# Optimization experiments

Hardware: AMD Instinct MI355X
Metric: run time of the kernel (lower is better)

## Reference

```python
import jax, jax.numpy as jnp
import numpy as np

N_QUBITS = 14
N_LAYERS = 4
BATCH = 2048
DIM = 2 ** N_QUBITS


def setup_inputs() -> dict:
    key = jax.random.key(0)
    k1, k2 = jax.random.split(key)
    x = jax.random.normal(k1, (BATCH, N_QUBITS), dtype=jnp.float32)
    params = 2.0 * jnp.pi * jax.random.uniform(k2, (N_LAYERS, 1, N_QUBITS), dtype=jnp.float32)
    return {"x": x, "params": params}


def _angle_embed_x(x):
    """RX(x_q) angle embedding from |0...0>: product state, qubit 0 most significant."""
    B, n = x.shape
    c = jnp.cos(x / 2)
    s = jnp.sin(x / 2)
    state = jnp.ones((B, 1), dtype=jnp.complex64)
    for q in range(n):  # fixed small loop over qubits (kron build-up)
        amp = jnp.stack([c[:, q] + 0j, (-1j) * s[:, q]], axis=-1).astype(jnp.complex64)  # (B,2)
        state = (state[:, :, None] * amp[:, None, :]).reshape(B, -1)
    return state  # (B, 2^n)


def _apply_rx(state, theta, q, n):
    """Apply RX(theta) on qubit q to batched state (B, 2^n)."""
    c = jnp.cos(theta / 2).astype(jnp.complex64)
    s = ((-1j) * jnp.sin(theta / 2)).astype(jnp.complex64)
    B = state.shape[0]
    st = state.reshape(B, 2 ** q, 2, 2 ** (n - q - 1))
    a0, a1 = st[:, :, 0, :], st[:, :, 1, :]
    new = jnp.stack([c * a0 + s * a1, s * a0 + c * a1], axis=2)
    return new.reshape(B, -1)


def _apply_cnot(state, ctrl, tgt, n):
    B = state.shape[0]
    lo, hi = min(ctrl, tgt), max(ctrl, tgt)
    st = state.reshape(B, 2 ** lo, 2, 2 ** (hi - lo - 1), 2, 2 ** (n - hi - 1))
    if ctrl < tgt:
        # control axis=2, target axis=4: flip target where control==1
        flipped = st[:, :, 1, :, ::-1, :]
        st = jnp.stack([st[:, :, 0], flipped], axis=2)
    else:
        # control axis=4, target axis=2
        flipped = st[:, :, ::-1, :, 1, :]
        st = jnp.stack([st[:, :, :, :, 0, :], flipped], axis=4)
    return st.reshape(B, -1)


def _z_signs(n):
    # sign[q, k] = +1 if bit q (MSB-first) of k is 0 else -1
    k = np.arange(2 ** n)
    bits = (k[None, :] >> np.arange(n - 1, -1, -1)[:, None]) & 1
    return jnp.asarray(1.0 - 2.0 * bits, dtype=jnp.float32)  # (n, 2^n)


def reference(x, params):
    n = N_QUBITS
    state = _angle_embed_x(x)  # (B, 2^n) complex64
    for layer in range(N_LAYERS):
        w = params[layer, 0]  # (n,)
        for q in range(n):
            state = _apply_rx(state, w[q], q, n)
        for q in range(n):  # ring of CNOTs (basic entangling layer)
            state = _apply_cnot(state, q, (q + 1) % n, n)
    probs = state.real ** 2 + state.imag ** 2  # (B, 2^n)
    return probs @ _z_signs(n).T  # (B, n) per-qubit <Z>
```

## Files before the change

### kernel.cpp

```cpp
#include <hip/hip_runtime.h>
#include <hip/hip_fp16.h>

#define NQ     14
#define NL     4
#define BATCH  2048
#define DIM    16384
#define BLK    512
#define NCH    (DIM / 4)
#define PCH    (NCH + NCH / 8)

using f2 = __attribute__((ext_vector_type(2))) float;
__device__ __forceinline__ f2 ff2(float a, float b) { f2 r; r.x = a; r.y = b; return r; }

__device__ __forceinline__ unsigned h2u(__half2 h) { return __builtin_bit_cast(unsigned, h); }
__device__ __forceinline__ __half2 u2h(unsigned u) { return __builtin_bit_cast(__half2, u); }
__device__ __forceinline__ unsigned sw16(unsigned u) { return __builtin_amdgcn_alignbit(u, u, 16); }

template <int K>
__device__ __forceinline__ void rot_k(__half2* X, __half2* Y, __half2 T, __half2 Sn) {
#pragma unroll
  for (int k = 0; k < 16; ++k) {
    if (!(k & K)) {
      const int k1 = k | K;
      const __half2 u1 = __hfma2(T, Y[k1], X[k]);
      const __half2 w1 = __hfma2(Sn, u1, Y[k1]);
      X[k]  = __hfma2(T, w1, u1);
      Y[k1] = w1;
      const __half2 u2 = __hfma2(T, Y[k], X[k1]);
      const __half2 w2 = __hfma2(Sn, u2, Y[k]);
      X[k1] = __hfma2(T, w2, u2);
      Y[k]  = w2;
    }
  }
}
__device__ __forceinline__ void rot0(__half2* X, __half2* Y, __half2 T, __half2 Sn) {
#pragma unroll
  for (int k = 0; k < 16; ++k) {
    const __half2 sy = __lowhigh2highlow(Y[k]);
    const __half2 u = __hfma2(T, sy, X[k]);
    const __half2 w = __hfma2(Sn, u, sy);
    X[k] = __hfma2(T, w, u);
    Y[k] = __lowhigh2highlow(w);
  }
}

__device__ __forceinline__ void cnot_scatter(char* sb, const int* offD, int P,
                                             const __half2* X, const __half2* Y) {
#pragma unroll
  for (int g = 0; g < 8; ++g) {
    const int k0 = 2 * g;
    const unsigned w0 = __builtin_amdgcn_perm(h2u(X[k0 ^ 12]), h2u(X[k0]), 0x07060100u);
    const unsigned w1 = __builtin_amdgcn_perm(h2u(Y[k0 ^ 12]), h2u(Y[k0]), 0x07060100u);
    const unsigned w2 = __builtin_amdgcn_perm(h2u(X[k0 ^ 13]), h2u(X[k0 ^ 1]), 0x05040302u);
    const unsigned w3 = __builtin_amdgcn_perm(h2u(Y[k0 ^ 13]), h2u(Y[k0 ^ 1]), 0x05040302u);
    const bool rev = ((P ^ (__popc(g) & 1)) != 0);
    const uint4 o = make_uint4(rev ? sw16(w2) : w0, rev ? sw16(w3) : w1,
                               rev ? sw16(w0) : w2, rev ? sw16(w1) : w3);
    *(uint4*)(sb + offD[g]) = o;
  }
}

__global__ __launch_bounds__(BLK)
__attribute__((amdgpu_waves_per_eu(4, 4)))
void qsim_kernel(const float* __restrict__ x,
                 const float* __restrict__ params,
                 float* __restrict__ out) {
  __shared__ uint4 lds[PCH];
  __shared__ float exc[NQ], exs[NQ];
  __shared__ uint2 gTS[NL * NQ];
  __shared__ float red[8][16];
  char* const sb = (char*)lds;

  const int b = blockIdx.x;
  const int t = threadIdx.x;

  if (t < NQ) {
    const float xv = x[b * NQ + t] + params[t];
    exc[t] = cosf(0.5f * xv); exs[t] = sinf(0.5f * xv);
  }
  if (t >= NQ && t < NL * NQ) {
    float ph = 0.5f * params[t];
    if (ph > 1.5707964f) ph -= 3.14159265f;
    const float tf = tanf(0.5f * ph);
    const __half th = __float2half_rn(tf);
    const float thf = __half2float(th);
    const float sf = 2.0f * thf / (1.0f + thf * thf);
    gTS[t] = make_uint2(h2u(__half2half2(th)), h2u(__float2half2_rn(-sf)));
  }
  __syncthreads();

  __half2 X[16], Y[16];

  char* const pA = sb + 16 * (9 * t);
  char* const pB = sb + 16 * (t & 7) + 1152 * (t >> 3);
  char* const pC = sb + 16 * ((t & 63) + ((t >> 3) & 7) + 576 * (t >> 6));
  char* const pD = sb + 16 * (t + (t >> 3));

  int MA0 = 0;
  {
    const int Me[9] = {0x2007, 0x200F, 0x201F, 0x203F, 0x207F, 0x20FF, 0x21FF, 0x23FF, 0x27FF};
#pragma unroll
    for (int i = 0; i < 9; ++i) if ((t >> i) & 1) MA0 ^= Me[i];
  }
  int offD[8];
#pragma unroll
  for (int g = 0; g < 8; ++g) {
    const int Mrep = ((g & 1) ? 0x2FFF : 0) ^ ((g & 2) ? 0x3FFF : 0) ^ ((g & 4) ? 0x1FFF : 0);
    const int cT = (MA0 ^ Mrep) >> 2;
    offD[g] = 16 * (cT + (cT >> 3));
  }
  const int P = __popc(t) & 1;

  {
    float pb = 1.0f;
#pragma unroll
    for (int i = 0; i < 9; ++i) pb *= ((t >> i) & 1) ? exs[11 - i] : exc[11 - i];
    const int pct = __popc(t);
#pragma unroll
    for (int m = 0; m < 8; ++m) {
      const float fm = ((m & 1) ? exs[2] : exc[2]) * ((m & 2) ? exs[1] : exc[1]) *
                       ((m & 4) ? exs[0] : exc[0]);
      float xv[4], yv[4];
#pragma unroll
      for (int l = 0; l < 4; ++l) {
        const float fl = ((l & 1) ? exs[13] : exc[13]) * ((l & 2) ? exs[12] : exc[12]);
        const float f = pb * fm * fl;
        const int pc = (pct + __popc(m) + __popc(l)) & 3;
        xv[l] = (pc == 0) ? f : ((pc == 2) ? -f : 0.0f);
        yv[l] = (pc == 1) ? -f : ((pc == 3) ? f : 0.0f);
      }
      X[2 * m]     = __floats2half2_rn(xv[0], xv[1]);
      X[2 * m + 1] = __floats2half2_rn(xv[2], xv[3]);
      Y[2 * m]     = __floats2half2_rn(yv[0], yv[1]);
      Y[2 * m + 1] = __floats2half2_rn(yv[2], yv[3]);
    }
  }
  cnot_scatter(sb, offD, P, X, Y);
  __syncthreads();

#pragma unroll
  for (int layer = 1; layer < NL; ++layer) {
    __half2 T, Sn;
#define MKST(qi) { const uint2 g_ = gTS[layer * NQ + (qi)]; T = u2h(g_.x); Sn = u2h(g_.y); }

#pragma unroll
    for (int i = 0; i < 8; ++i) {
      const uint4 u = *(const uint4*)(pA + 16 * i);
      X[2 * i] = u2h(u.x); Y[2 * i] = u2h(u.y);
      X[2 * i + 1] = u2h(u.z); Y[2 * i + 1] = u2h(u.w);
    }
    MKST(13); rot0(X, Y, T, Sn);
    MKST(12); rot_k<1>(X, Y, T, Sn);
    MKST(11); rot_k<2>(X, Y, T, Sn);
    MKST(10); rot_k<4>(X, Y, T, Sn);
    MKST(9);  rot_k<8>(X, Y, T, Sn);
#pragma unroll
    for (int i = 0; i < 8; ++i)
      *(uint4*)(pA + 16 * i) = make_uint4(h2u(X[2 * i]), h2u(Y[2 * i]),
                                          h2u(X[2 * i + 1]), h2u(Y[2 * i + 1]));
    __builtin_amdgcn_wave_barrier();

#pragma unroll
    for (int m = 0; m < 8; ++m) {
      const uint4 u = *(const uint4*)(pB + 144 * m);
      X[2 * m] = u2h(u.x); Y[2 * m] = u2h(u.y);
      X[2 * m + 1] = u2h(u.z); Y[2 * m + 1] = u2h(u.w);
    }
    MKST(8); rot_k<2>(X, Y, T, Sn);
    MKST(7); rot_k<4>(X, Y, T, Sn);
    MKST(6); rot_k<8>(X, Y, T, Sn);
#pragma unroll
    for (int m = 0; m < 8; ++m)
      *(uint4*)(pB + 144 * m) = make_uint4(h2u(X[2 * m]), h2u(Y[2 * m]),
                                           h2u(X[2 * m + 1]), h2u(Y[2 * m + 1]));
    __builtin_amdgcn_wave_barrier();

#pragma unroll
    for (int m = 0; m < 8; ++m) {
      const uint4 u = *(const uint4*)(pC + 1152 * m);
      X[2 * m] = u2h(u.x); Y[2 * m] = u2h(u.y);
      X[2 * m + 1] = u2h(u.z); Y[2 * m + 1] = u2h(u.w);
    }
    MKST(5); rot_k<2>(X, Y, T, Sn);
    MKST(4); rot_k<4>(X, Y, T, Sn);
    MKST(3); rot_k<8>(X, Y, T, Sn);
#pragma unroll
    for (int m = 0; m < 8; ++m)
      *(uint4*)(pC + 1152 * m) = make_uint4(h2u(X[2 * m]), h2u(Y[2 * m]),
                                            h2u(X[2 * m + 1]), h2u(Y[2 * m + 1]));
    __syncthreads();

#pragma unroll
    for (int m = 0; m < 8; ++m) {
      const uint4 u = *(const uint4*)(pD + 9216 * m);
      X[2 * m] = u2h(u.x); Y[2 * m] = u2h(u.y);
      X[2 * m + 1] = u2h(u.z); Y[2 * m + 1] = u2h(u.w);
    }
    if (layer < NL - 1) __syncthreads();
    MKST(2); rot_k<2>(X, Y, T, Sn);
    MKST(1); rot_k<4>(X, Y, T, Sn);
    MKST(0); rot_k<8>(X, Y, T, Sn);
#undef MKST

    if (layer < NL - 1) {
      cnot_scatter(sb, offD, P, X, Y);
      __syncthreads();
    }
  }

  {
    f2 pp[16];
#pragma unroll
    for (int k = 0; k < 16; ++k) {
      const float xl = __low2float(X[k]), xh = __high2float(X[k]);
      const float yl = __low2float(Y[k]), yh = __high2float(Y[k]);
      pp[k] = ff2(fmaf(xl, xl, yl * yl), fmaf(xh, xh, yh * yh));
    }
#pragma unroll
    for (int st = 0; st < 4; ++st) {
      const int h = 1 << st;
#pragma unroll
      for (int k = 0; k < 16; ++k) {
        if (!(k & h)) {
          const f2 u = pp[k], w = pp[k | h];
          pp[k] = u + w;
          pp[k | h] = u - w;
        }
      }
    }
    float w24 = pp[12].x + pp[12].y;
    float w28 = pp[14].x + pp[14].y;
    float w30 = pp[15].x + pp[15].y;
    float w31 = pp[15].x - pp[15].y;
    float w15 = pp[7].x - pp[7].y;

    const int lane = t & 63;
#pragma unroll
    for (int m = 0; m < 6; ++m) {
      const int h = 1 << m;
      const bool hi = (lane & h) != 0;
      float u;
      u = __shfl_xor(w28, h, 64); w28 = hi ? (u - w28) : (u + w28);
      u = __shfl_xor(w30, h, 64); w30 = hi ? (u - w30) : (u + w30);
      u = __shfl_xor(w31, h, 64); w31 = hi ? (u - w31) : (u + w31);
      u = __shfl_xor(w15, h, 64); w15 = hi ? (u - w15) : (u + w15);
      u = __shfl_xor(w24, h, 64); w24 = u + w24;
    }
    const int w = t >> 6;
    const float swv = (__popc(w) & 1) ? -1.0f : 1.0f;
    if (lane == 0) {
      red[w][1] = w24;
      red[w][2] = w28;
      red[w][3] = ((w >> 2) & 1) ? -w28 : w28;
      red[w][4] = (((w >> 1) ^ (w >> 2)) & 1) ? -w28 : w28;
      red[w][5] = swv * w28;
    } else if (lane == 32) { red[w][6]  = swv * w28; }
    else if (lane == 48)   { red[w][7]  = swv * w28; }
    else if (lane == 56)   { red[w][8]  = swv * w28; }
    else if (lane == 60)   { red[w][9]  = swv * w28; }
    else if (lane == 62)   { red[w][10] = swv * w28; }
    else if (lane == 63)   { red[w][11] = swv * w28;
                             red[w][12] = swv * w30;
                             red[w][13] = swv * w31;
                             red[w][0]  = swv * w15; }
    __syncthreads();
    if (t < NQ) {
      float sq = 0.0f;
#pragma unroll
      for (int ww = 0; ww < 8; ++ww) sq += red[ww][t];
      out[b * NQ + t] = sq;
    }
  }
}

extern "C" void kernel_launch(void* const* d_in, const int* in_sizes, int n_in,
                              void* d_out, int out_size, void* d_ws, size_t ws_size,
                              hipStream_t stream) {
  const float* x      = (const float*)d_in[0];
  const float* params = (const float*)d_in[1];
  float* out          = (float*)d_out;
  qsim_kernel<<<BATCH, BLK, 0, stream>>>(x, params, out);
}
```

Measured before the change: 163.3 us.

## Replace per-qubit RX half2 rotations with grouped-qubit MFMA unitary matmuls

A small prep kernel builds fused 32x32 and 16x16 complex unitaries, as split real and imaginary fp16 parts, for groups of 5, 5 and 4 RX gates per layer and writes them to the workspace. The main kernel now applies each group as MFMA matrix multiplies over the LDS-resident state, in a new swizzled 64KB LDS layout with the CNOT permutation folded into the scatter addresses. The aim is to move the rotation arithmetic from packed-half VALU work onto matrix cores. In exchange it adds a second launch, larger LDS use per block, and rounds the fused unitaries to fp16, which may change accuracy.

```diff
diff --git a/kernel.cpp b/kernel.cpp
--- a/kernel.cpp
+++ b/kernel.cpp
@@ -1,275 +1,320 @@
 #include <hip/hip_runtime.h>
 #include <hip/hip_fp16.h>
+#include <stdint.h>
 
 #define NQ     14
 #define NL     4
 #define BATCH  2048
 #define DIM    16384
-#define BLK    512
-#define NCH    (DIM / 4)
-#define PCH    (NCH + NCH / 8)
-
-using f2 = __attribute__((ext_vector_type(2))) float;
-__device__ __forceinline__ f2 ff2(float a, float b) { f2 r; r.x = a; r.y = b; return r; }
-
-__device__ __forceinline__ unsigned h2u(__half2 h) { return __builtin_bit_cast(unsigned, h); }
-__device__ __forceinline__ __half2 u2h(unsigned u) { return __builtin_bit_cast(__half2, u); }
-__device__ __forceinline__ unsigned sw16(unsigned u) { return __builtin_amdgcn_alignbit(u, u, 16); }
-
-template <int K>
-__device__ __forceinline__ void rot_k(__half2* X, __half2* Y, __half2 T, __half2 Sn) {
-#pragma unroll
-  for (int k = 0; k < 16; ++k) {
-    if (!(k & K)) {
-      const int k1 = k | K;
-      const __half2 u1 = __hfma2(T, Y[k1], X[k]);
-      const __half2 w1 = __hfma2(Sn, u1, Y[k1]);
-      X[k]  = __hfma2(T, w1, u1);
-      Y[k1] = w1;
-      const __half2 u2 = __hfma2(T, Y[k], X[k1]);
-      const __half2 w2 = __hfma2(Sn, u2, Y[k]);
-      X[k1] = __hfma2(T, w2, u2);
-      Y[k]  = w2;
+
+using half8  = __attribute__((ext_vector_type(8)))  _Float16;
+using half4  = __attribute__((ext_vector_type(4)))  _Float16;
+using f32x16 = __attribute__((ext_vector_type(16))) float;
+using f32x4  = __attribute__((ext_vector_type(4)))  float;
+
+constexpr uint32_t mmask(int b) { return b < 13 ? (((1u << (b + 1)) - 1u) | 0x2000u) : 0x1FFFu; }
+constexpr uint32_t laddr(uint32_t a) {
+  return ((a >> 5) << 7) ^ (((((a >> 2) & 7u) ^ ((a >> 5) & 7u)) & 7u) << 4) ^ ((a & 3u) << 2);
+}
+constexpr uint32_t IMG(int b) { return laddr(mmask(b)); }
+
+struct TabEmb { uint32_t v[32]; constexpr TabEmb() : v() {
+  for (int k = 0; k < 32; ++k) { uint32_t x = 0;
+    for (int b = 0; b < 5; ++b) if ((k >> b) & 1) x ^= IMG(b); v[k] = x; } } };
+constexpr TabEmb EMBT{};
+
+struct TabSc { uint32_t v[8][4]; constexpr TabSc() : v() {
+  for (int i = 0; i < 8; ++i) for (int r = 0; r < 4; ++r) { uint32_t x = 0;
+    if (r & 1) x ^= IMG(0); if (r & 2) x ^= IMG(1);
+    if (i & 1) x ^= IMG(4); if (i & 2) x ^= IMG(5); if (i & 4) x ^= IMG(6);
+    v[i][r] = x; } } };
+constexpr TabSc SCT{};
+
+struct TabEc { uint32_t v[16]; constexpr TabEc() : v() {
+  for (int e = 0; e < 16; ++e) { uint32_t ce = (uint32_t)((e & 3) | ((e >> 2) << 3));
+    v[e] = (ce << 6) ^ (((ce ^ (ce >> 2)) & 3u) << 4); } } };
+constexpr TabEc ECT{};
+
+__device__ __forceinline__ half8 h8(uint32_t a, uint32_t b, uint32_t c, uint32_t d) {
+  union { uint32_t u[4]; half8 h; } z; z.u[0]=a; z.u[1]=b; z.u[2]=c; z.u[3]=d; return z.h; }
+__device__ __forceinline__ half4 h4v(uint32_t a, uint32_t b) {
+  union { uint32_t u[2]; half4 h; } z; z.u[0]=a; z.u[1]=b; return z.h; }
+__device__ __forceinline__ uint4 ld16(const char* p) {
+  return *(const uint4*)__builtin_assume_aligned(p, 16); }
+__device__ __forceinline__ void st16(char* p, uint4 v) {
+  *(uint4*)__builtin_assume_aligned(p, 16) = v; }
+__device__ __forceinline__ uint32_t pkh2(float a, float b) {
+  return __builtin_bit_cast(uint32_t, __floats2half2_rn(a, b)); }
+
+__global__ void uprep_kernel(const float* __restrict__ params, __half* __restrict__ U) {
+  const int id = blockIdx.x * 256 + threadIdx.x;
+  int li, grp, r, k, nb, off, mstride;
+  if (id < 6144) { li = id >> 11; const int sub = id & 2047;
+    grp = sub >> 10; const int cell = sub & 1023; r = cell >> 5; k = cell & 31; nb = 5;
+    off = li * 4608 + grp * 2048 + r * 32 + k; mstride = 1024; }
+  else { const int id2 = id - 6144; li = id2 >> 8; const int cell = id2 & 255;
+    grp = 2; r = cell >> 4; k = cell & 15; nb = 4;
+    off = li * 4608 + 4096 + r * 16 + k; mstride = 256; }
+  const float* th = params + (li + 1) * NQ;
+  float mag = 1.f; int d = 0;
+  for (int j = 0; j < nb; ++j) {
+    const int pbit = (grp == 0) ? j : (grp == 1) ? 5 + j : 10 + j;
+    const float ph = 0.5f * th[13 - pbit];
+    const int df = ((r >> j) ^ (k >> j)) & 1;
+    mag *= df ? sinf(ph) : cosf(ph);
+    d += df;
+  }
+  float R = 0.f, I = 0.f;
+  switch (d & 3) { case 0: R = mag; break; case 1: I = -mag; break;
+                   case 2: R = -mag; break; default: I = mag; break; }
+  U[off] = __float2half_rn(R);
+  U[off + mstride] = __float2half_rn(I);
+}
+
+__global__ __launch_bounds__(512)
+__attribute__((amdgpu_waves_per_eu(4, 4)))
+void qsim_kernel(const float* __restrict__ x, const float* __restrict__ params,
+                 const __half* __restrict__ U, float* __restrict__ out) {
+  __shared__ uint32_t lds[DIM];
+  __shared__ float red[8][16];
+  __shared__ float exc[NQ], exs[NQ];
+  char* const sb = (char*)lds;
+
+  const int b = blockIdx.x;
+  const int t = threadIdx.x;
+  const int w = t >> 6, l = t & 63;
+  const int hi = l >> 5, l31 = l & 31, l15 = l & 15, h4 = (l >> 4) & 3;
+  const int swz = l & 7;
+
+  if (t < NQ) { const float xv = x[b * NQ + t] + params[t];
+                exc[t] = cosf(0.5f * xv); exs[t] = sinf(0.5f * xv); }
+  __syncthreads();
+
+  const uint32_t colAB = (uint32_t)(((w << 6) | l31) << 7);
+  const uint32_t sgl = (uint32_t)(((l15 ^ (l15 >> 2)) ^ w) & 3);
+  const uint32_t gcr = (uint32_t)((w << 13) | (l15 << 6) | (((h4 ^ (int)sgl) & 3) << 4));
+  const uint32_t lbc = ((uint32_t)l31 << 11) ^ ((uint32_t)hi << 8)
+      ^ ((uint32_t)(((w >> 1) ^ ((l31 >> 2) & 3) ^ hi) & 3) << 4)
+      ^ ((uint32_t)(((w << 1) ^ l) & 3) << 2);
+  uint32_t scb = 0;
+  { if (l & 16) scb ^= IMG(2);
+    if (l & 32) scb ^= IMG(3);
+#pragma unroll
+    for (int j = 0; j < 4; ++j) if ((l15 >> j) & 1) scb ^= IMG(10 + j);
+#pragma unroll
+    for (int j = 0; j < 3; ++j) if ((w >> j) & 1) scb ^= IMG(7 + j); }
+
+  {
+    float pb = 1.f;
+#pragma unroll
+    for (int j = 0; j < 9; ++j) pb *= ((t >> j) & 1) ? exs[8 - j] : exc[8 - j];
+    uint32_t eb = 0;
+#pragma unroll
+    for (int j = 0; j < 9; ++j) if ((t >> j) & 1) eb ^= IMG(5 + j);
+    float fm[8], fl[4];
+#pragma unroll
+    for (int m = 0; m < 8; ++m)
+      fm[m] = ((m & 1) ? exs[11] : exc[11]) * ((m & 2) ? exs[10] : exc[10]) * ((m & 4) ? exs[9] : exc[9]);
+#pragma unroll
+    for (int m = 0; m < 4; ++m)
+      fl[m] = ((m & 1) ? exs[13] : exc[13]) * ((m & 2) ? exs[12] : exc[12]);
+    const int pct = __popc(t);
+#pragma unroll
+    for (int k = 0; k < 32; ++k) {
+      const float f = pb * fm[k >> 2] * fl[k & 3];
+      const int pc = (pct + __popc(k)) & 3;
+      const float xr = (pc == 0) ? f : ((pc == 2) ? -f : 0.f);
+      const float yi = (pc == 1) ? -f : ((pc == 3) ? f : 0.f);
+      *(uint32_t*)(sb + (eb ^ EMBT.v[k])) = pkh2(xr, yi);
     }
   }
-}
-__device__ __forceinline__ void rot0(__half2* X, __half2* Y, __half2 T, __half2 Sn) {
-#pragma unroll
-  for (int k = 0; k < 16; ++k) {
-    const __half2 sy = __lowhigh2highlow(Y[k]);
-    const __half2 u = __hfma2(T, sy, X[k]);
-    const __half2 w = __hfma2(Sn, u, sy);
-    X[k] = __hfma2(T, w, u);
-    Y[k] = __lowhigh2highlow(w);
-  }
-}
-
-__device__ __forceinline__ void cnot_scatter(char* sb, const int* offD, int P,
-                                             const __half2* X, const __half2* Y) {
-#pragma unroll
-  for (int g = 0; g < 8; ++g) {
-    const int k0 = 2 * g;
-    const unsigned w0 = __builtin_amdgcn_perm(h2u(X[k0 ^ 12]), h2u(X[k0]), 0x07060100u);
-    const unsigned w1 = __builtin_amdgcn_perm(h2u(Y[k0 ^ 12]), h2u(Y[k0]), 0x07060100u);
-    const unsigned w2 = __builtin_amdgcn_perm(h2u(X[k0 ^ 13]), h2u(X[k0 ^ 1]), 0x05040302u);
-    const unsigned w3 = __builtin_amdgcn_perm(h2u(Y[k0 ^ 13]), h2u(Y[k0 ^ 1]), 0x05040302u);
-    const bool rev = ((P ^ (__popc(g) & 1)) != 0);
-    const uint4 o = make_uint4(rev ? sw16(w2) : w0, rev ? sw16(w3) : w1,
-                               rev ? sw16(w0) : w2, rev ? sw16(w1) : w3);
-    *(uint4*)(sb + offD[g]) = o;
-  }
-}
-
-__global__ __launch_bounds__(BLK)
-__attribute__((amdgpu_waves_per_eu(4, 4)))
-void qsim_kernel(const float* __restrict__ x,
-                 const float* __restrict__ params,
-                 float* __restrict__ out) {
-  __shared__ uint4 lds[PCH];
-  __shared__ float exc[NQ], exs[NQ];
-  __shared__ uint2 gTS[NL * NQ];
-  __shared__ float red[8][16];
-  char* const sb = (char*)lds;
-
-  const int b = blockIdx.x;
-  const int t = threadIdx.x;
-
-  if (t < NQ) {
-    const float xv = x[b * NQ + t] + params[t];
-    exc[t] = cosf(0.5f * xv); exs[t] = sinf(0.5f * xv);
-  }
-  if (t >= NQ && t < NL * NQ) {
-    float ph = 0.5f * params[t];
-    if (ph > 1.5707964f) ph -= 3.14159265f;
-    const float tf = tanf(0.5f * ph);
-    const __half th = __float2half_rn(tf);
-    const float thf = __half2float(th);
-    const float sf = 2.0f * thf / (1.0f + thf * thf);
-    gTS[t] = make_uint2(h2u(__half2half2(th)), h2u(__float2half2_rn(-sf)));
-  }
   __syncthreads();
 
-  __half2 X[16], Y[16];
-
-  char* const pA = sb + 16 * (9 * t);
-  char* const pB = sb + 16 * (t & 7) + 1152 * (t >> 3);
-  char* const pC = sb + 16 * ((t & 63) + ((t >> 3) & 7) + 576 * (t >> 6));
-  char* const pD = sb + 16 * (t + (t >> 3));
-
-  int MA0 = 0;
-  {
-    const int Me[9] = {0x2007, 0x200F, 0x201F, 0x203F, 0x207F, 0x20FF, 0x21FF, 0x23FF, 0x27FF};
-#pragma unroll
-    for (int i = 0; i < 9; ++i) if ((t >> i) & 1) MA0 ^= Me[i];
-  }
-  int offD[8];
-#pragma unroll
-  for (int g = 0; g < 8; ++g) {
-    const int Mrep = ((g & 1) ? 0x2FFF : 0) ^ ((g & 2) ? 0x3FFF : 0) ^ ((g & 4) ? 0x1FFF : 0);
-    const int cT = (MA0 ^ Mrep) >> 2;
-    offD[g] = 16 * (cT + (cT >> 3));
-  }
-  const int P = __popc(t) & 1;
-
-  {
-    float pb = 1.0f;
-#pragma unroll
-    for (int i = 0; i < 9; ++i) pb *= ((t >> i) & 1) ? exs[11 - i] : exc[11 - i];
-    const int pct = __popc(t);
-#pragma unroll
-    for (int m = 0; m < 8; ++m) {
-      const float fm = ((m & 1) ? exs[2] : exc[2]) * ((m & 2) ? exs[1] : exc[1]) *
-                       ((m & 4) ? exs[0] : exc[0]);
-      float xv[4], yv[4];
-#pragma unroll
-      for (int l = 0; l < 4; ++l) {
-        const float fl = ((l & 1) ? exs[13] : exc[13]) * ((l & 2) ? exs[12] : exc[12]);
-        const float f = pb * fm * fl;
-        const int pc = (pct + __popc(m) + __popc(l)) & 3;
-        xv[l] = (pc == 0) ? f : ((pc == 2) ? -f : 0.0f);
-        yv[l] = (pc == 1) ? -f : ((pc == 3) ? f : 0.0f);
-      }
-      X[2 * m]     = __floats2half2_rn(xv[0], xv[1]);
-      X[2 * m + 1] = __floats2half2_rn(xv[2], xv[3]);
-      Y[2 * m]     = __floats2half2_rn(yv[0], yv[1]);
-      Y[2 * m + 1] = __floats2half2_rn(yv[2], yv[3]);
+#pragma unroll 1
+  for (int li = 0; li < 3; ++li) {
+    const __half* Ul = U + li * 4608;
+
+    {
+      half8 bR[2], bI[2];
+#pragma unroll
+      for (int s = 0; s < 2; ++s) {
+        const __half* up = Ul + l31 * 32 + s * 16 + hi * 8;
+        bR[s] = *(const half8*)__builtin_assume_aligned(up, 16);
+        bI[s] = *(const half8*)__builtin_assume_aligned(up + 1024, 16);
+      }
+#pragma unroll
+      for (int n = 0; n < 2; ++n) {
+        const uint32_t cb = colAB + (uint32_t)(n << 12);
+        f32x16 cX = {}, cY = {};
+#pragma unroll
+        for (int s = 0; s < 2; ++s) {
+          const uint4 q0 = ld16(sb + cb + (uint32_t)((((s << 2) + (hi << 1) + 0) ^ swz) << 4));
+          const uint4 q1 = ld16(sb + cb + (uint32_t)((((s << 2) + (hi << 1) + 1) ^ swz) << 4));
+          const uint32_t dw[8] = {q0.x, q0.y, q0.z, q0.w, q1.x, q1.y, q1.z, q1.w};
+          uint32_t ax[4], ay[4], an[4];
+#pragma unroll
+          for (int j = 0; j < 4; ++j) {
+            ax[j] = __builtin_amdgcn_perm(dw[2 * j + 1], dw[2 * j], 0x05040100u);
+            ay[j] = __builtin_amdgcn_perm(dw[2 * j + 1], dw[2 * j], 0x07060302u);
+            an[j] = ay[j] ^ 0x80008000u;
+          }
+          const half8 aX = h8(ax[0], ax[1], ax[2], ax[3]);
+          const half8 aY = h8(ay[0], ay[1], ay[2], ay[3]);
+          const half8 aN = h8(an[0], an[1], an[2], an[3]);
+          cX = __builtin_amdgcn_mfma_f32_32x32x16_f16(aX, bR[s], cX, 0, 0, 0);
+          cX = __builtin_amdgcn_mfma_f32_32x32x16_f16(aN, bI[s], cX, 0, 0, 0);
+          cY = __builtin_amdgcn_mfma_f32_32x32x16_f16(aX, bI[s], cY, 0, 0, 0);
+          cY = __builtin_amdgcn_mfma_f32_32x32x16_f16(aY, bR[s], cY, 0, 0, 0);
+        }
+#pragma unroll
+        for (int u = 0; u < 4; ++u) {
+          uint4 o;
+          o.x = pkh2(cX[4 * u + 0], cY[4 * u + 0]); o.y = pkh2(cX[4 * u + 1], cY[4 * u + 1]);
+          o.z = pkh2(cX[4 * u + 2], cY[4 * u + 2]); o.w = pkh2(cX[4 * u + 3], cY[4 * u + 3]);
+          st16(sb + cb + (uint32_t)((((u << 1) + hi) ^ swz) << 4), o);
+        }
+      }
+      __builtin_amdgcn_wave_barrier();
+    }
+
+    {
+      half8 bR[2], bI[2];
+#pragma unroll
+      for (int s = 0; s < 2; ++s) {
+        const __half* up = Ul + 2048 + l31 * 32 + s * 16 + hi * 8;
+        bR[s] = *(const half8*)__builtin_assume_aligned(up, 16);
+        bI[s] = *(const half8*)__builtin_assume_aligned(up + 1024, 16);
+      }
+      uint4 dr[2][2][2];
+#pragma unroll
+      for (int n = 0; n < 2; ++n)
+#pragma unroll
+        for (int s = 0; s < 2; ++s)
+#pragma unroll
+          for (int j = 0; j < 2; ++j)
+            dr[n][s][j] = ld16(sb + colAB + (uint32_t)(n << 12)
+                               + (uint32_t)((((s << 2) + (hi << 1) + j) ^ swz) << 4));
+      __syncthreads();
+#pragma unroll
+      for (int n = 0; n < 2; ++n) {
+        f32x16 cX = {}, cY = {};
+#pragma unroll
+        for (int s = 0; s < 2; ++s) {
+          const uint32_t dw[8] = {dr[n][s][0].x, dr[n][s][0].y, dr[n][s][0].z, dr[n][s][0].w,
+                                  dr[n][s][1].x, dr[n][s][1].y, dr[n][s][1].z, dr[n][s][1].w};
+          uint32_t ax[4], ay[4], an[4];
+#pragma unroll
+          for (int j = 0; j < 4; ++j) {
+            ax[j] = __builtin_amdgcn_perm(dw[2 * j + 1], dw[2 * j], 0x05040100u);
+            ay[j] = __builtin_amdgcn_perm(dw[2 * j + 1], dw[2 * j], 0x07060302u);
+            an[j] = ay[j] ^ 0x80008000u;
+          }
+          const half8 aX = h8(ax[0], ax[1], ax[2], ax[3]);
+          const half8 aY = h8(ay[0], ay[1], ay[2], ay[3]);
+          const half8 aN = h8(an[0], an[1], an[2], an[3]);
+          cX = __builtin_amdgcn_mfma_f32_32x32x16_f16(aX, bR[s], cX, 0, 0, 0);
+          cX = __builtin_amdgcn_mfma_f32_32x32x16_f16(aN, bI[s], cX, 0, 0, 0);
+          cY = __builtin_amdgcn_mfma_f32_32x32x16_f16(aX, bI[s], cY, 0, 0, 0);
+          cY = __builtin_amdgcn_mfma_f32_32x32x16_f16(aY, bR[s], cY, 0, 0, 0);
+        }
+        const uint32_t lb = lbc ^ (uint32_t)(n << 2);
+#pragma unroll
+        for (int e = 0; e < 16; ++e)
+          *(uint32_t*)(sb + (lb ^ ECT.v[e])) = pkh2(cX[e], cY[e]);
+      }
+      __syncthreads();
+    }
+
+    {
+      const __half* up = Ul + 4096 + l15 * 16 + h4 * 4;
+      const half4 bR = *(const half4*)__builtin_assume_aligned(up, 8);
+      const half4 bI = *(const half4*)__builtin_assume_aligned(up + 256, 8);
+      uint4 dc[8];
+#pragma unroll
+      for (int i = 0; i < 8; ++i)
+        dc[i] = ld16(sb + gcr + (uint32_t)(i << 10));
+      __syncthreads();
+      float sE0[8], sE1[8], sE2[8];
+#pragma unroll
+      for (int i = 0; i < 8; ++i) {
+        const int m2 = (i >> 1) & 3;
+        const uint32_t ph[4] = {dc[i].x, dc[i].y, dc[i].z, dc[i].w};
+        const uint32_t d0 = ph[0 ^ m2], d1 = ph[1 ^ m2], d2 = ph[2 ^ m2], d3 = ph[3 ^ m2];
+        const uint32_t x0 = __builtin_amdgcn_perm(d1, d0, 0x05040100u);
+        const uint32_t x1 = __builtin_amdgcn_perm(d3, d2, 0x05040100u);
+        const uint32_t y0 = __builtin_amdgcn_perm(d1, d0, 0x07060302u);
+        const uint32_t y1 = __builtin_amdgcn_perm(d3, d2, 0x07060302u);
+        const half4 aX = h4v(x0, x1);
+        const half4 aY = h4v(y0, y1);
+        const half4 aN = h4v(y0 ^ 0x80008000u, y1 ^ 0x80008000u);
+        f32x4 cX = {}, cY = {};
+        cX = __builtin_amdgcn_mfma_f32_16x16x16f16(aX, bR, cX, 0, 0, 0);
+        cX = __builtin_amdgcn_mfma_f32_16x16x16f16(aN, bI, cX, 0, 0, 0);
+        cY = __builtin_amdgcn_mfma_f32_16x16x16f16(aX, bI, cY, 0, 0, 0);
+        cY = __builtin_amdgcn_mfma_f32_16x16x16f16(aY, bR, cY, 0, 0, 0);
+        if (li < 2) {
+#pragma unroll
+          for (int r = 0; r < 4; ++r)
+            *(uint32_t*)(sb + (scb ^ SCT.v[i][r])) = pkh2(cX[r], cY[r]);
+        } else {
+          const float p0 = fmaf(cX[0], cX[0], cY[0] * cY[0]);
+          const float p1 = fmaf(cX[1], cX[1], cY[1] * cY[1]);
+          const float p2 = fmaf(cX[2], cX[2], cY[2] * cY[2]);
+          const float p3 = fmaf(cX[3], cX[3], cY[3] * cY[3]);
+          const float t01 = p0 + p1, t23 = p2 + p3;
+          const float d01 = p0 - p1, d23 = p2 - p3;
+          sE0[i] = t01 + t23;
+          sE1[i] = t01 - t23;
+          sE2[i] = d01 - d23;
+        }
+      }
+      if (li < 2) {
+        __syncthreads();
+      } else {
+        float A = 0.f, Bv = 0.f, Cv = 0.f;
+#pragma unroll
+        for (int i = 0; i < 8; ++i) {
+          if (__popc(i) & 1) { A -= sE2[i]; Bv -= sE1[i]; Cv -= sE0[i]; }
+          else               { A += sE2[i]; Bv += sE1[i]; Cv += sE0[i]; }
+        }
+        const float u0 = sE0[0] + sE0[1], u1 = sE0[2] + sE0[3];
+        const float u2 = sE0[4] + sE0[5], u3 = sE0[6] + sE0[7];
+        float Dv = (u0 - u1) - (u2 - u3);
+        float Ev = (u0 + u1) - (u2 + u3);
+        float Fv = (u0 + u1) + (u2 + u3);
+#pragma unroll
+        for (int m = 0; m < 6; ++m) {
+          const int hb = 1 << m;
+          const bool up2 = (l & hb) != 0;
+          float u;
+          u = __shfl_xor(A, hb, 64);  A  = up2 ? (u - A)  : (u + A);
+          u = __shfl_xor(Bv, hb, 64); Bv = up2 ? (u - Bv) : (u + Bv);
+          u = __shfl_xor(Cv, hb, 64); Cv = up2 ? (u - Cv) : (u + Cv);
+          u = __shfl_xor(Dv, hb, 64); Dv = up2 ? (u - Dv) : (u + Dv);
+          u = __shfl_xor(Ev, hb, 64); Ev = up2 ? (u - Ev) : (u + Ev);
+          u = __shfl_xor(Fv, hb, 64); Fv = up2 ? (u - Fv) : (u + Fv);
+        }
+        const float swv = (__popc(w) & 1) ? -1.f : 1.f;
+        if (l == 63)      { red[w][13] = swv * A; red[w][12] = swv * Bv; red[w][11] = swv * Cv; }
+        else if (l == 55) { red[w][0]  = swv * A; }
+        else if (l == 47) { red[w][10] = swv * Cv; }
+        else if (l == 15) { red[w][9] = swv * Cv; red[w][8] = swv * Dv; red[w][7] = swv * Ev;
+                            red[w][6] = swv * Fv;
+                            red[w][5] = (__popc(w >> 1) & 1) ? -Fv : Fv;
+                            red[w][4] = ((w >> 2) & 1) ? -Fv : Fv;
+                            red[w][3] = Fv; }
+        else if (l == 14) { red[w][2] = Fv; }
+        else if (l == 12) { red[w][1] = Fv; }
+      }
     }
   }
-  cnot_scatter(sb, offD, P, X, Y);
+
   __syncthreads();
-
-#pragma unroll
-  for (int layer = 1; layer < NL; ++layer) {
-    __half2 T, Sn;
-#define MKST(qi) { const uint2 g_ = gTS[layer * NQ + (qi)]; T = u2h(g_.x); Sn = u2h(g_.y); }
-
-#pragma unroll
-    for (int i = 0; i < 8; ++i) {
-      const uint4 u = *(const uint4*)(pA + 16 * i);
-      X[2 * i] = u2h(u.x); Y[2 * i] = u2h(u.y);
-      X[2 * i + 1] = u2h(u.z); Y[2 * i + 1] = u2h(u.w);
-    }
-    MKST(13); rot0(X, Y, T, Sn);
-    MKST(12); rot_k<1>(X, Y, T, Sn);
-    MKST(11); rot_k<2>(X, Y, T, Sn);
-    MKST(10); rot_k<4>(X, Y, T, Sn);
-    MKST(9);  rot_k<8>(X, Y, T, Sn);
-#pragma unroll
-    for (int i = 0; i < 8; ++i)
-      *(uint4*)(pA + 16 * i) = make_uint4(h2u(X[2 * i]), h2u(Y[2 * i]),
-                                          h2u(X[2 * i + 1]), h2u(Y[2 * i + 1]));
-    __builtin_amdgcn_wave_barrier();
-
-#pragma unroll
-    for (int m = 0; m < 8; ++m) {
-      const uint4 u = *(const uint4*)(pB + 144 * m);
-      X[2 * m] = u2h(u.x); Y[2 * m] = u2h(u.y);
-      X[2 * m + 1] = u2h(u.z); Y[2 * m + 1] = u2h(u.w);
-    }
-    MKST(8); rot_k<2>(X, Y, T, Sn);
-    MKST(7); rot_k<4>(X, Y, T, Sn);
-    MKST(6); rot_k<8>(X, Y, T, Sn);
-#pragma unroll
-    for (int m = 0; m < 8; ++m)
-      *(uint4*)(pB + 144 * m) = make_uint4(h2u(X[2 * m]), h2u(Y[2 * m]),
-                                           h2u(X[2 * m + 1]), h2u(Y[2 * m + 1]));
-    __builtin_amdgcn_wave_barrier();
-
-#pragma unroll
-    for (int m = 0; m < 8; ++m) {
-      const uint4 u = *(const uint4*)(pC + 1152 * m);
-      X[2 * m] = u2h(u.x); Y[2 * m] = u2h(u.y);
-      X[2 * m + 1] = u2h(u.z); Y[2 * m + 1] = u2h(u.w);
-    }
-    MKST(5); rot_k<2>(X, Y, T, Sn);
-    MKST(4); rot_k<4>(X, Y, T, Sn);
-    MKST(3); rot_k<8>(X, Y, T, Sn);
-#pragma unroll
-    for (int m = 0; m < 8; ++m)
-      *(uint4*)(pC + 1152 * m) = make_uint4(h2u(X[2 * m]), h2u(Y[2 * m]),
-                                            h2u(X[2 * m + 1]), h2u(Y[2 * m + 1]));
-    __syncthreads();
-
-#pragma unroll
-    for (int m = 0; m < 8; ++m) {
-      const uint4 u = *(const uint4*)(pD + 9216 * m);
-      X[2 * m] = u2h(u.x); Y[2 * m] = u2h(u.y);
-      X[2 * m + 1] = u2h(u.z); Y[2 * m + 1] = u2h(u.w);
-    }
-    if (layer < NL - 1) __syncthreads();
-    MKST(2); rot_k<2>(X, Y, T, Sn);
-    MKST(1); rot_k<4>(X, Y, T, Sn);
-    MKST(0); rot_k<8>(X, Y, T, Sn);
-#undef MKST
-
-    if (layer < NL - 1) {
-      cnot_scatter(sb, offD, P, X, Y);
-      __syncthreads();
-    }
-  }
-
-  {
-    f2 pp[16];
-#pragma unroll
-    for (int k = 0; k < 16; ++k) {
-      const float xl = __low2float(X[k]), xh = __high2float(X[k]);
-      const float yl = __low2float(Y[k]), yh = __high2float(Y[k]);
-      pp[k] = ff2(fmaf(xl, xl, yl * yl), fmaf(xh, xh, yh * yh));
-    }
-#pragma unroll
-    for (int st = 0; st < 4; ++st) {
-      const int h = 1 << st;
-#pragma unroll
-      for (int k = 0; k < 16; ++k) {
-        if (!(k & h)) {
-          const f2 u = pp[k], w = pp[k | h];
-          pp[k] = u + w;
-          pp[k | h] = u - w;
-        }
-      }
-    }
-    float w24 = pp[12].x + pp[12].y;
-    float w28 = pp[14].x + pp[14].y;
-    float w30 = pp[15].x + pp[15].y;
-    float w31 = pp[15].x - pp[15].y;
-    float w15 = pp[7].x - pp[7].y;
-
-    const int lane = t & 63;
-#pragma unroll
-    for (int m = 0; m < 6; ++m) {
-      const int h = 1 << m;
-      const bool hi = (lane & h) != 0;
-      float u;
-      u = __shfl_xor(w28, h, 64); w28 = hi ? (u - w28) : (u + w28);
-      u = __shfl_xor(w30, h, 64); w30 = hi ? (u - w30) : (u + w30);
-      u = __shfl_xor(w31, h, 64); w31 = hi ? (u - w31) : (u + w31);
-      u = __shfl_xor(w15, h, 64); w15 = hi ? (u - w15) : (u + w15);
-      u = __shfl_xor(w24, h, 64); w24 = u + w24;
-    }
-    const int w = t >> 6;
-    const float swv = (__popc(w) & 1) ? -1.0f : 1.0f;
-    if (lane == 0) {
-      red[w][1] = w24;
-      red[w][2] = w28;
-      red[w][3] = ((w >> 2) & 1) ? -w28 : w28;
-      red[w][4] = (((w >> 1) ^ (w >> 2)) & 1) ? -w28 : w28;
-      red[w][5] = swv * w28;
-    } else if (lane == 32) { red[w][6]  = swv * w28; }
-    else if (lane == 48)   { red[w][7]  = swv * w28; }
-    else if (lane == 56)   { red[w][8]  = swv * w28; }
-    else if (lane == 60)   { red[w][9]  = swv * w28; }
-    else if (lane == 62)   { red[w][10] = swv * w28; }
-    else if (lane == 63)   { red[w][11] = swv * w28;
-                             red[w][12] = swv * w30;
-                             red[w][13] = swv * w31;
-                             red[w][0]  = swv * w15; }
-    __syncthreads();
-    if (t < NQ) {
-      float sq = 0.0f;
-#pragma unroll
-      for (int ww = 0; ww < 8; ++ww) sq += red[ww][t];
-      out[b * NQ + t] = sq;
-    }
+  if (t < NQ) {
+    float sq = 0.f;
+#pragma unroll
+    for (int ww = 0; ww < 8; ++ww) sq += red[ww][t];
+    out[b * NQ + t] = sq;
   }
 }
 
@@ -279,5 +324,7 @@
   const float* x      = (const float*)d_in[0];
   const float* params = (const float*)d_in[1];
   float* out          = (float*)d_out;
-  qsim_kernel<<<BATCH, BLK, 0, stream>>>(x, params, out);
+  __half* U           = (__half*)d_ws;
+  uprep_kernel<<<27, 256, 0, stream>>>(params, U);
+  qsim_kernel<<<BATCH, 512, 0, stream>>>(x, params, (const __half*)U, out);
 }
```

Result: faster. 157.6 us (-3.5%).
